# Optimization experiments

Measured on AMD Instinct MI355X. Metric: run time of the kernel, lower is better.

## Reference

```python
import jax, jax.numpy as jnp
import numpy as np
from jax import lax

B_, L_, D_MODEL, D_FF = 8, 1024, 512, 2048
D_STATE, D_CONV, EXPAND = 16, 4, 2
D_IN = EXPAND * D_MODEL
DT_RANK = (D_MODEL + 15) // 16  # 32


def _ln(x, g, b, eps=1e-5):
    m = jnp.mean(x, -1, keepdims=True)
    v = jnp.var(x, -1, keepdims=True)
    return (x - m) / jnp.sqrt(v + eps) * g + b


def _selective_scan(u, dt, A, Bm, Cm, D):
    # u, dt: (B,L,d_in); Bm, Cm: (B,L,d_state); A: (d_in,d_state); D: (d_in,)
    def step(h, xs):
        dt_t, B_t, C_t, u_t = xs  # (B,d_in),(B,ds),(B,ds),(B,d_in)
        dA = jnp.exp(dt_t[..., None] * A)                       # (B,d_in,ds)
        h = dA * h + (dt_t * u_t)[..., None] * B_t[:, None, :]  # (B,d_in,ds)
        y = jnp.einsum('bds,bs->bd', h, C_t)
        return h, y

    h0 = jnp.zeros((u.shape[0], D_IN, D_STATE), u.dtype)
    xs = (dt.transpose(1, 0, 2), Bm.transpose(1, 0, 2),
          Cm.transpose(1, 0, 2), u.transpose(1, 0, 2))
    _, ys = lax.scan(step, h0, xs)           # (L,B,d_in)
    return ys.transpose(1, 0, 2) + u * D


def _mamba(x, in_w, conv_w, conv_b, xp_w, dtp_w, dtp_b, A_log, D, out_w):
    xz = x @ in_w.T                              # (B,L,2*d_in)
    xs, z = jnp.split(xz, 2, axis=-1)
    # causal depthwise conv1d over L
    xc = lax.conv_general_dilated(xs.transpose(0, 2, 1), conv_w, (1,),
                                  [(D_CONV - 1, 0)], feature_group_count=D_IN)
    xc = jax.nn.silu(xc + conv_b[None, :, None]).transpose(0, 2, 1)  # (B,L,d_in)
    x_dbl = xc @ xp_w.T
    dt, Bm, Cm = jnp.split(x_dbl, [DT_RANK, DT_RANK + D_STATE], axis=-1)
    dt = jax.nn.softplus(dt @ dtp_w.T + dtp_b)
    A = -jnp.exp(A_log)
    y = _selective_scan(xc, dt, A, Bm, Cm, D)
    y = y * jax.nn.silu(z)
    return y @ out_w.T


def _forward(x,
             in1_w, conv1d1_w, conv1d1_b, xp1_w, dtp1_w, dtp1_b, Alog1, D1, outp1_w,
             in2_w, conv1d2_w, conv1d2_b, xp2_w, dtp2_w, dtp2_b, Alog2, D2, outp2_w,
             c1_w, c1_b, c2_w, c2_b, ln1_g, ln1_b, ln2_g, ln2_b):
    x_res = x  # dropout is identity in eval
    fwd = _mamba(x, in1_w, conv1d1_w, conv1d1_b, xp1_w, dtp1_w, dtp1_b, Alog1, D1, outp1_w)
    bwd = _mamba(jnp.flip(x, 1), in2_w, conv1d2_w, conv1d2_b, xp2_w, dtp2_w, dtp2_b,
                 Alog2, D2, outp2_w)
    new_x = fwd + jnp.flip(bwd, 1)
    x = _ln(new_x + x_res, ln1_g, ln1_b)
    y = jax.nn.gelu(jnp.einsum('bld,fd->blf', x, c1_w[:, :, 0]) + c1_b, approximate=False)
    y = jnp.einsum('blf,df->bld', y, c2_w[:, :, 0]) + c2_b
    return _ln(x + y, ln2_g, ln2_b)


def setup_inputs() -> dict:
    key = jax.random.key(0)
    ks = iter(jax.random.split(key, 32))
    rn = lambda shape, s=0.02: jax.random.normal(next(ks), shape, jnp.float32) * s

    def mamba_params():
        return dict(in_w=rn((2 * D_IN, D_MODEL)), conv_w=rn((D_IN, 1, D_CONV)),
                    conv_b=rn((D_IN,)), xp_w=rn((DT_RANK + 2 * D_STATE, D_IN)),
                    dtp_w=rn((D_IN, DT_RANK)), dtp_b=rn((D_IN,)),
                    A_log=jnp.log(jnp.tile(jnp.arange(1., D_STATE + 1.), (D_IN, 1))).astype(jnp.float32),
                    D=jnp.ones((D_IN,), jnp.float32), out_w=rn((D_MODEL, D_IN)))

    m1, m2 = mamba_params(), mamba_params()
    return {
        'x': jax.random.normal(next(ks), (B_, L_, D_MODEL), jnp.float32),
        'in1_w': m1['in_w'], 'conv1d1_w': m1['conv_w'], 'conv1d1_b': m1['conv_b'],
        'xp1_w': m1['xp_w'], 'dtp1_w': m1['dtp_w'], 'dtp1_b': m1['dtp_b'],
        'Alog1': m1['A_log'], 'D1': m1['D'], 'outp1_w': m1['out_w'],
        'in2_w': m2['in_w'], 'conv1d2_w': m2['conv_w'], 'conv1d2_b': m2['conv_b'],
        'xp2_w': m2['xp_w'], 'dtp2_w': m2['dtp_w'], 'dtp2_b': m2['dtp_b'],
        'Alog2': m2['A_log'], 'D2': m2['D'], 'outp2_w': m2['out_w'],
        'c1_w': rn((D_FF, D_MODEL, 1)), 'c1_b': rn((D_FF,)),
        'c2_w': rn((D_MODEL, D_FF, 1)), 'c2_b': rn((D_MODEL,)),
        'ln1_g': jnp.ones((D_MODEL,), jnp.float32), 'ln1_b': jnp.zeros((D_MODEL,), jnp.float32),
        'ln2_g': jnp.ones((D_MODEL,), jnp.float32), 'ln2_b': jnp.zeros((D_MODEL,), jnp.float32),
    }


def reference(x,
              in1_w, conv1d1_w, conv1d1_b, xp1_w, dtp1_w, dtp1_b, Alog1, D1, outp1_w,
              in2_w, conv1d2_w, conv1d2_b, xp2_w, dtp2_w, dtp2_b, Alog2, D2, outp2_w,
              c1_w, c1_b, c2_w, c2_b, ln1_g, ln1_b, ln2_g, ln2_b):
    return _forward(x,
                    in1_w, conv1d1_w, conv1d1_b, xp1_w, dtp1_w, dtp1_b, Alog1, D1, outp1_w,
                    in2_w, conv1d2_w, conv1d2_b, xp2_w, dtp2_w, dtp2_b, Alog2, D2, outp2_w,
                    c1_w, c1_b, c2_w, c2_b, ln1_g, ln1_b, ln2_g, ln2_b)
```

## Files before the change

kernel.cpp:

```cpp
#include <hip/hip_runtime.h>
#include <hip/hip_bf16.h>
#include <math.h>

#define B_SZ 8
#define L_SZ 1024
#define DM 512
#define DFF 2048
#define DIN 1024
#define DSTATE 16
#define DTRANK 32
#define MROWS (B_SZ * L_SZ)
#define CH 256
#define NCH 4

typedef __hip_bfloat16 bf16;
typedef unsigned short u16;
using f32x4 = __attribute__((ext_vector_type(4))) float;
using bfrag = __attribute__((ext_vector_type(8))) short;

__device__ inline float ldf(const float* p, long i) { return p[i]; }
__device__ inline float ldf(const bf16* p, long i) {
  return __uint_as_float((unsigned)((const u16*)p)[i] << 16);
}
__device__ inline void stf(float* p, long i, float v) { p[i] = v; }
__device__ inline void stf(bf16* p, long i, float v) { p[i] = __float2bfloat16(v); }
__device__ inline float b2f(u16 x) {
  return __uint_as_float((unsigned)x << 16);
}
__device__ inline u16 f2b(float v) {
  union { bf16 h; u16 u; } c;
  c.h = __float2bfloat16(v);
  return c.u;
}

__device__ inline float fexp2(float x) {
  float r;
  asm("v_exp_f32 %0, %1" : "=v"(r) : "v"(x));
  return r;
}

typedef __attribute__((address_space(1))) const void g_void;
typedef __attribute__((address_space(3))) void l_void;
__device__ inline void gl_lds16(const void* g, void* l) {
  __builtin_amdgcn_global_load_lds((g_void*)g, (l_void*)l, 16, 0, 0);
}

__device__ inline float4 ld4f_bt(const float* p) { return *(const float4*)p; }
__device__ inline float4 ld4f_bt(const bf16* p) {
  ushort4 u = *(const ushort4*)p;
  float4 v;
  v.x = b2f(u.x); v.y = b2f(u.y); v.z = b2f(u.z); v.w = b2f(u.w);
  return v;
}

__device__ inline void ld16f(const float* p, uint4& lo, uint4& hi) {
  float4 a = *(const float4*)p, b = *(const float4*)(p + 4);
  float4 c = *(const float4*)(p + 8), d = *(const float4*)(p + 12);
  union { uint4 v; u16 s[8]; } L, H;
  L.s[0] = f2b(a.x); L.s[1] = f2b(a.y); L.s[2] = f2b(a.z); L.s[3] = f2b(a.w);
  L.s[4] = f2b(b.x); L.s[5] = f2b(b.y); L.s[6] = f2b(b.z); L.s[7] = f2b(b.w);
  H.s[0] = f2b(c.x); H.s[1] = f2b(c.y); H.s[2] = f2b(c.z); H.s[3] = f2b(c.w);
  H.s[4] = f2b(d.x); H.s[5] = f2b(d.y); H.s[6] = f2b(d.z); H.s[7] = f2b(d.w);
  lo = L.v; hi = H.v;
}

__device__ inline float dpp_add_r8(float x) {
  float r; asm("v_add_f32 %0, %1, %2 row_ror:8" : "=v"(r) : "v"(x), "v"(x)); return r;
}
__device__ inline float dpp_add_r4(float x) {
  float r; asm("v_add_f32 %0, %1, %2 row_ror:4" : "=v"(r) : "v"(x), "v"(x)); return r;
}
__device__ inline float dpp_add_r2(float x) {
  float r; asm("v_add_f32 %0, %1, %2 row_ror:2" : "=v"(r) : "v"(x), "v"(x)); return r;
}
__device__ inline float dpp_add_r1(float x) {
  float r; asm("v_add_f32 %0, %1, %2 row_ror:1" : "=v"(r) : "v"(x), "v"(x)); return r;
}
__device__ inline float row16_sum(float x) {
  return dpp_add_r1(dpp_add_r2(dpp_add_r4(dpp_add_r8(x))));
}

__device__ inline int flipL(int r) {
  int t = r & (L_SZ - 1);
  return (r - t) + (L_SZ - 1 - t);
}

__global__ __launch_bounds__(256) void cvt8_k(
    const float* s0, const float* s1, const float* s2, const float* s3,
    const float* s4, const float* s5, const float* s6, const float* s7,
    bf16* d0, bf16* d1, bf16* d2, bf16* d3,
    bf16* d4, bf16* d5, bf16* d6, bf16* d7) {
  int blk = blockIdx.x;
  const float* s; bf16* d; long off;
  if (blk < 2048)       { s = s0; d = d0; off = (long)blk * 256; }
  else if (blk < 4096)  { s = s1; d = d1; off = (long)(blk - 2048) * 256; }
  else if (blk < 6144)  { s = s2; d = d2; off = (long)(blk - 4096) * 256; }
  else if (blk < 8192)  { s = s3; d = d3; off = (long)(blk - 6144) * 256; }
  else if (blk < 10240) { s = s4; d = d4; off = (long)(blk - 8192) * 256; }
  else if (blk < 12288) { s = s5; d = d5; off = (long)(blk - 10240) * 256; }
  else if (blk < 16384) { s = s6; d = d6; off = (long)(blk - 12288) * 256; }
  else                  { s = s7; d = d7; off = (long)(blk - 16384) * 256; }
  off += threadIdx.x;
  d[off] = __float2bfloat16(s[off]);
}

constexpr int MEPI_STORE2 = 0;
constexpr int MEPI_GATE2 = 1;
constexpr int MEPI_BIAS_GELU = 2;
constexpr int MEPI_BIAS_RES = 3;

template <int EPI, typename TA, typename TO>
__global__ __launch_bounds__(256) void mgemm_k(
    const TA* __restrict__ Ab, int lda,
    const bf16* __restrict__ Wb, int ldw,
    TO* __restrict__ C, TO* __restrict__ C2, int ldc,
    const float* __restrict__ bias,
    const float* __restrict__ res,
    int K) {
  constexpr bool ABF = (sizeof(TA) == 2);
  __shared__ u16 Wsm[128][32];
  __shared__ u16 AsmL[ABF ? 128 : 1][32];
  __shared__ u16 AsmP[ABF ? 1 : 128][ABF ? 1 : 40];
  const int tid = threadIdx.x;
  const int m0 = blockIdx.y * 128;
  const int n0 = blockIdx.x * 128;

  const int srow4 = tid >> 2;
  const int q16 = tid & 3;
  const u16* Wg0 = (const u16*)Wb + (long)(n0 + srow4) * ldw + q16 * 8;
  const u16* Wg1 = (const u16*)Wb + (long)(n0 + 64 + srow4) * ldw + q16 * 8;
  char* WsmB = (char*)&Wsm[0][0] + (tid >> 6) * 1024;

  const u16* Ag0 = (const u16*)Ab + (long)(m0 + srow4) * lda + q16 * 8;
  const u16* Ag1 = (const u16*)Ab + (long)(m0 + 64 + srow4) * lda + q16 * 8;
  char* AsmB = (char*)&AsmL[0][0] + (tid >> 6) * 1024;

  const int srow = tid >> 1;
  const int scol = (tid & 1) * 16;
  const TA* Agf = Ab + (long)(m0 + srow) * lda + scol;

  const int lane = tid & 63, quad = lane >> 4, l16 = lane & 15;
  const int wid = tid >> 6;
  const int wm = (wid & 1) * 64, wn = (wid >> 1) * 64;

  f32x4 acc[4][4];
#pragma unroll
  for (int i = 0; i < 4; ++i)
#pragma unroll
    for (int j = 0; j < 4; ++j) acc[i][j] = {0.f, 0.f, 0.f, 0.f};

  for (int k0 = 0; k0 < K; k0 += 32) {
    uint4 av0, av1;
    if constexpr (!ABF) ld16f((const float*)(Agf + k0), av0, av1);
    __syncthreads();
    gl_lds16(Wg0 + k0, WsmB);
    gl_lds16(Wg1 + k0, WsmB + 4096);
    if constexpr (ABF) {
      gl_lds16(Ag0 + k0, AsmB);
      gl_lds16(Ag1 + k0, AsmB + 4096);
    } else {
      *(uint4*)&AsmP[srow][scol] = av0;
      *(uint4*)&AsmP[srow][scol + 8] = av1;
    }
    __syncthreads();
    bfrag a[4], b[4];
#pragma unroll
    for (int mi = 0; mi < 4; ++mi) {
      if constexpr (ABF)
        a[mi] = *(const bfrag*)&AsmL[wm + mi * 16 + l16][quad * 8];
      else
        a[mi] = *(const bfrag*)&AsmP[wm + mi * 16 + l16][quad * 8];
    }
#pragma unroll
    for (int ni = 0; ni < 4; ++ni)
      b[ni] = *(const bfrag*)&Wsm[wn + ni * 16 + l16][quad * 8];
#pragma unroll
    for (int mi = 0; mi < 4; ++mi)
#pragma unroll
      for (int ni = 0; ni < 4; ++ni)
        acc[mi][ni] = __builtin_amdgcn_mfma_f32_16x16x32_bf16(
            a[mi], b[ni], acc[mi][ni], 0, 0, 0);
  }

  const bool second = (n0 >= DIN);
#pragma unroll
  for (int mi = 0; mi < 4; ++mi)
#pragma unroll
    for (int ni = 0; ni < 4; ++ni)
#pragma unroll
      for (int r = 0; r < 4; ++r) {
        int row = m0 + wm + mi * 16 + quad * 4 + r;
        int col = n0 + wn + ni * 16 + l16;
        float v = acc[mi][ni][r];
        if (EPI == MEPI_STORE2) {
          if (second) stf(C2, (long)flipL(row) * ldc + (col - DIN), v);
          else stf(C, (long)row * ldc + col, v);
        } else if (EPI == MEPI_GATE2) {
          TO* T = second ? C2 : C;
          long oi = second ? ((long)flipL(row) * ldc + (col - DIN))
                           : ((long)row * ldc + col);
          float y = ldf((const bf16*)T, oi);
          float sz = v / (1.f + __expf(-v));
          stf(T, oi, y * sz);
        } else if (EPI == MEPI_BIAS_GELU) {
          long oi = (long)row * ldc + col;
          v += bias[col];
          v = 0.5f * v * (1.f + erff(v * 0.70710678118654752440f));
          stf(C, oi, v);
        } else if (EPI == MEPI_BIAS_RES) {
          long oi = (long)row * ldc + col;
          ((float*)C)[oi] = v + bias[col] + res[oi];
        }
      }
}

__global__ __launch_bounds__(256) void mmerge_k(
    const bf16* __restrict__ y1, const bf16* __restrict__ y2,
    const bf16* __restrict__ W1, const bf16* __restrict__ W2,
    const float* __restrict__ xres, float* __restrict__ newx) {
  __shared__ u16 AsmL[128][32];
  __shared__ u16 Wsm[128][32];
  const int tid = threadIdx.x;
  const int m0 = blockIdx.y * 128;
  const int n0 = blockIdx.x * 128;

  const int srow4 = tid >> 2;
  const int q16 = tid & 3;
  int r1a = m0 + srow4, r1b = m0 + 64 + srow4;
  int r2a = flipL(r1a), r2b = flipL(r1b);
  const u16* A1g0 = (const u16*)y1 + (long)r1a * DIN + q16 * 8;
  const u16* A1g1 = (const u16*)y1 + (long)r1b * DIN + q16 * 8;
  const u16* A2g0 = (const u16*)y2 + (long)r2a * DIN + q16 * 8;
  const u16* A2g1 = (const u16*)y2 + (long)r2b * DIN + q16 * 8;
  const u16* W1g0 = (const u16*)W1 + (long)(n0 + srow4) * DIN + q16 * 8;
  const u16* W1g1 = (const u16*)W1 + (long)(n0 + 64 + srow4) * DIN + q16 * 8;
  const u16* W2g0 = (const u16*)W2 + (long)(n0 + srow4) * DIN + q16 * 8;
  const u16* W2g1 = (const u16*)W2 + (long)(n0 + 64 + srow4) * DIN + q16 * 8;
  char* AsmB = (char*)&AsmL[0][0] + (tid >> 6) * 1024;
  char* WsmB = (char*)&Wsm[0][0] + (tid >> 6) * 1024;

  const int lane = tid & 63, quad = lane >> 4, l16 = lane & 15;
  const int wid = tid >> 6;
  const int wm = (wid & 1) * 64, wn = (wid >> 1) * 64;

  f32x4 acc[4][4];
#pragma unroll
  for (int i = 0; i < 4; ++i)
#pragma unroll
    for (int j = 0; j < 4; ++j) acc[i][j] = {0.f, 0.f, 0.f, 0.f};

  for (int k0 = 0; k0 < 2 * DIN; k0 += 32) {
    const bool ph2 = (k0 >= DIN);
    const int kk = k0 & (DIN - 1);
    const u16* a0 = ph2 ? A2g0 : A1g0;
    const u16* a1 = ph2 ? A2g1 : A1g1;
    const u16* w0 = ph2 ? W2g0 : W1g0;
    const u16* w1 = ph2 ? W2g1 : W1g1;
    __syncthreads();
    gl_lds16(a0 + kk, AsmB);
    gl_lds16(a1 + kk, AsmB + 4096);
    gl_lds16(w0 + kk, WsmB);
    gl_lds16(w1 + kk, WsmB + 4096);
    __syncthreads();
    bfrag a[4], b[4];
#pragma unroll
    for (int mi = 0; mi < 4; ++mi)
      a[mi] = *(const bfrag*)&AsmL[wm + mi * 16 + l16][quad * 8];
#pragma unroll
    for (int ni = 0; ni < 4; ++ni)
      b[ni] = *(const bfrag*)&Wsm[wn + ni * 16 + l16][quad * 8];
#pragma unroll
    for (int mi = 0; mi < 4; ++mi)
#pragma unroll
      for (int ni = 0; ni < 4; ++ni)
        acc[mi][ni] = __builtin_amdgcn_mfma_f32_16x16x32_bf16(
            a[mi], b[ni], acc[mi][ni], 0, 0, 0);
  }

#pragma unroll
  for (int mi = 0; mi < 4; ++mi)
#pragma unroll
    for (int ni = 0; ni < 4; ++ni)
#pragma unroll
      for (int r = 0; r < 4; ++r) {
        int row = m0 + wm + mi * 16 + quad * 4 + r;
        int col = n0 + wn + ni * 16 + l16;
        long oi = (long)row * DM + col;
        newx[oi] = acc[mi][ni][r] + xres[oi];
      }
}

constexpr int EPI_NONE = 0;
constexpr int EPI_SOFTPLUS_ROW = 1;

#define BM 64
#define BN 64
#define BKK 16

template <int EPI, typename TB, typename TO>
__global__ __launch_bounds__(256) void gemmBT_k(
    const float* __restrict__ A,
    const TB* __restrict__ B,
    TO* __restrict__ C, int N,
    const float* __restrict__ bias, int K) {
  __shared__ float As[BKK][BM + 4];
  __shared__ float Bs[BKK][BN + 4];
  const int tid = threadIdx.x;
  const int m0 = blockIdx.y * BM;
  const int n0 = blockIdx.x * BN;
  const int tx = tid & 15;
  const int ty = tid >> 4;
  const int lrow = tid >> 2;
  const int lcol = (tid & 3) * 4;
  const int kr = tid >> 4;
  const int nc = (tid & 15) * 4;

  const float* Arow = A + (long)(m0 + lrow) * K;

  float acc[4][4] = {};
  for (int k0 = 0; k0 < K; k0 += BKK) {
    float4 av = *(const float4*)(Arow + k0 + lcol);
    float4 bv = ld4f_bt(B + (long)(k0 + kr) * N + n0 + nc);
    As[lcol + 0][lrow] = av.x; As[lcol + 1][lrow] = av.y;
    As[lcol + 2][lrow] = av.z; As[lcol + 3][lrow] = av.w;
    Bs[kr][nc + 0] = bv.x; Bs[kr][nc + 1] = bv.y;
    Bs[kr][nc + 2] = bv.z; Bs[kr][nc + 3] = bv.w;
    __syncthreads();
#pragma unroll
    for (int k = 0; k < BKK; ++k) {
      float a[4], b[4];
#pragma unroll
      for (int i = 0; i < 4; ++i) a[i] = As[k][ty * 4 + i];
#pragma unroll
      for (int j = 0; j < 4; ++j) b[j] = Bs[k][tx * 4 + j];
#pragma unroll
      for (int i = 0; i < 4; ++i)
#pragma unroll
        for (int j = 0; j < 4; ++j) acc[i][j] += a[i] * b[j];
    }
    __syncthreads();
  }

#pragma unroll
  for (int i = 0; i < 4; ++i) {
    int r = m0 + ty * 4 + i;
#pragma unroll
    for (int j = 0; j < 4; ++j) {
      int c = n0 + tx * 4 + j;
      float v = acc[i][j];
      if (EPI == EPI_SOFTPLUS_ROW) {
        v += bias[r];
        v = (v > 20.f) ? v : log1pf(__expf(v));
      }
      stf(C, (long)r * N + c, v);
    }
  }
}

#define XSLICE 4
#define XSZ ((long)64 * MROWS)

__global__ __launch_bounds__(256) void xprojs_k(
    const float* __restrict__ A1, const bf16* __restrict__ B1,
    float* __restrict__ P1,
    const float* __restrict__ A2, const bf16* __restrict__ B2,
    float* __restrict__ P2) {
  __shared__ float As[BKK][BM + 4];
  __shared__ float Bs[BKK][BN + 4];
  const int tid = threadIdx.x;
  const int n0 = blockIdx.x * BN;
  const int slice = blockIdx.y;
  const int kbeg = slice * (DIN / XSLICE);
  const int dir = blockIdx.z;
  const float* A = dir ? A2 : A1;
  const bf16* Bm = dir ? B2 : B1;
  float* P = (dir ? P2 : P1) + (long)slice * XSZ;
  const int N = MROWS, K = DIN;
  const int tx = tid & 15;
  const int ty = tid >> 4;
  const int lrow = tid >> 2;
  const int lcol = (tid & 3) * 4;
  const int kr = tid >> 4;
  const int nc = (tid & 15) * 4;

  const float* Arow = A + (long)lrow * K;

  float acc[4][4] = {};
  for (int k0 = kbeg; k0 < kbeg + DIN / XSLICE; k0 += BKK) {
    float4 av = *(const float4*)(Arow + k0 + lcol);
    float4 bv = ld4f_bt(Bm + (long)(k0 + kr) * N + n0 + nc);
    As[lcol + 0][lrow] = av.x; As[lcol + 1][lrow] = av.y;
    As[lcol + 2][lrow] = av.z; As[lcol + 3][lrow] = av.w;
    Bs[kr][nc + 0] = bv.x; Bs[kr][nc + 1] = bv.y;
    Bs[kr][nc + 2] = bv.z; Bs[kr][nc + 3] = bv.w;
    __syncthreads();
#pragma unroll
    for (int k = 0; k < BKK; ++k) {
      float a[4], b[4];
#pragma unroll
      for (int i = 0; i < 4; ++i) a[i] = As[k][ty * 4 + i];
#pragma unroll
      for (int j = 0; j < 4; ++j) b[j] = Bs[k][tx * 4 + j];
#pragma unroll
      for (int i = 0; i < 4; ++i)
#pragma unroll
        for (int j = 0; j < 4; ++j) acc[i][j] += a[i] * b[j];
    }
    __syncthreads();
  }

#pragma unroll
  for (int i = 0; i < 4; ++i) {
    int r = ty * 4 + i;
#pragma unroll
    for (int j = 0; j < 4; ++j) {
      int c = n0 + tx * 4 + j;
      P[(long)r * N + c] = acc[i][j];
    }
  }
}

__global__ __launch_bounds__(256) void xred_k(
    const float* __restrict__ P1, float* __restrict__ o1,
    const float* __restrict__ P2, float* __restrict__ o2) {
  long i = (long)blockIdx.x * 256 + threadIdx.x;
  const float* P = blockIdx.y ? P2 : P1;
  float* o = blockIdx.y ? o2 : o1;
  o[i] = P[i] + P[i + XSZ] + P[i + 2 * XSZ] + P[i + 3 * XSZ];
}

__global__ __launch_bounds__(256) void convT_k(
    const bf16* __restrict__ xs, const float* __restrict__ w,
    const float* __restrict__ b, bf16* __restrict__ xcT) {
  __shared__ u16 T[64][72];
  int c0 = blockIdx.x * 64;
  int r0 = blockIdx.y * 64;
  int tid = threadIdx.x;
  int tr = tid >> 2;
  int tc = (tid & 3) * 16;

  const u16* src = (const u16*)xs + (long)(r0 + tr) * DIN + c0 + tc;
  uint4 v0 = *(const uint4*)src;
  uint4 v1 = *(const uint4*)(src + 8);
  u16 tmp[16];
  *(uint4*)tmp = v0;
  *(uint4*)(tmp + 8) = v1;
#pragma unroll
  for (int j = 0; j < 16; ++j) T[tc + j][tr + 3] = tmp[j];
  bool head = (r0 & (L_SZ - 1)) == 0;
  if (tid < 12) {
    int hr = tid >> 2;
    int seg = (tid & 3) * 16;
    if (head) {
#pragma unroll
      for (int j = 0; j < 16; ++j) T[seg + j][hr] = 0;
    } else {
      const u16* hs = (const u16*)xs + (long)(r0 - 3 + hr) * DIN + c0 + seg;
      uint4 h0 = *(const uint4*)hs;
      uint4 h1 = *(const uint4*)(hs + 8);
      u16 ht[16];
      *(uint4*)ht = h0;
      *(uint4*)(ht + 8) = h1;
#pragma unroll
      for (int j = 0; j < 16; ++j) T[seg + j][hr] = ht[j];
    }
  }
  __syncthreads();

  int d = c0 + tr;
  float w0 = w[d * 4 + 0], w1 = w[d * 4 + 1], w2 = w[d * 4 + 2], w3 = w[d * 4 + 3];
  float bd = b[d];
  float X[19];
#pragma unroll
  for (int k = 0; k < 19; ++k) X[k] = b2f(T[tr][tc + k]);
  u16 o[16];
#pragma unroll
  for (int j = 0; j < 16; ++j) {
    float acc = bd + w0 * X[j] + w1 * X[j + 1] + w2 * X[j + 2] + w3 * X[j + 3];
    o[j] = f2b(acc / (1.f + __expf(-acc)));
  }
  u16* dst = (u16*)xcT + (long)d * MROWS + r0 + tc;
  *(uint4*)dst = *(uint4*)o;
  *(uint4*)(dst + 8) = *(uint4*)(o + 8);
}

__global__ __launch_bounds__(256, 4) void scan1_k(
    const u16* __restrict__ dtT1, const u16* __restrict__ dtT2,
    const u16* __restrict__ uT1, const u16* __restrict__ uT2,
    const float* __restrict__ xd1, const float* __restrict__ xd2,
    const float* __restrict__ Alog1, const float* __restrict__ Alog2,
    bf16* __restrict__ hl1, bf16* __restrict__ hl2,
    float* __restrict__ sd1, float* __restrict__ sd2) {
  int blk = blockIdx.x;
  int dblk = blk & 15;
  int r = blk >> 4;
  int c = r % 3; r /= 3;
  int b = r & 7;
  int dir = r >> 3;
  int tid = threadIdx.x;
  int s = tid & 15;
  int gi = tid >> 4;
  int d0 = dblk * 64 + gi * 4;
  const u16* dtT = dir ? dtT2 : dtT1;
  const u16* uT = dir ? uT2 : uT1;
  const float* xd = dir ? xd2 : xd1;
  const float* Alog = dir ? Alog2 : Alog1;
  bf16* hl = dir ? hl2 : hl1;
  float* sd = dir ? sd2 : sd1;

  float A2[4], h[4], sdt[4];
#pragma unroll
  for (int dd = 0; dd < 4; ++dd) {
    A2[dd] = -__expf(Alog[(d0 + dd) * DSTATE + s]) * 1.4426950408889634f;
    h[dd] = 0.f;
    sdt[dd] = 0.f;
  }
  long t0 = (long)b * L_SZ + c * CH;
  const u16* pdt = dtT + (long)d0 * MROWS + t0;
  const u16* pu = uT + (long)d0 * MROWS + t0;
  const float* pB = xd + (long)(DTRANK + s) * MROWS + t0;

  for (int g = 0; g < CH / 8; ++g) {
    union { uint4 v; u16 a[8]; } dt8[4], u8[4];
    union { float4 v[2]; float a[8]; } B8;
#pragma unroll
    for (int dd = 0; dd < 4; ++dd) {
      dt8[dd].v = *(const uint4*)(pdt + (long)dd * MROWS + g * 8);
      u8[dd].v = *(const uint4*)(pu + (long)dd * MROWS + g * 8);
    }
    B8.v[0] = *(const float4*)(pB + g * 8);
    B8.v[1] = *(const float4*)(pB + g * 8 + 4);
#pragma unroll
    for (int j = 0; j < 8; ++j) {
      float Bj = B8.a[j];
#pragma unroll
      for (int dd = 0; dd < 4; ++dd) {
        float dtv = b2f(dt8[dd].a[j]);
        float uv = b2f(u8[dd].a[j]);
        float da = fexp2(dtv * A2[dd]);
        h[dd] = da * h[dd] + (dtv * uv) * Bj;
        sdt[dd] += dtv;
      }
    }
  }
#pragma unroll
  for (int dd = 0; dd < 4; ++dd) {
    int ci = (b * 3 + c) * 1024 + d0 + dd;
    hl[(long)ci * 16 + s] = __float2bfloat16(h[dd]);
    if (s == 0) sd[ci] = sdt[dd];
  }
}

__global__ __launch_bounds__(256, 4) void scan2_k(
    const u16* __restrict__ dtT1, const u16* __restrict__ dtT2,
    const u16* __restrict__ uT1, const u16* __restrict__ uT2,
    const float* __restrict__ xd1, const float* __restrict__ xd2,
    const float* __restrict__ Alog1, const float* __restrict__ Alog2,
    const float* __restrict__ D1, const float* __restrict__ D2,
    const bf16* __restrict__ hl1, const bf16* __restrict__ hl2,
    const float* __restrict__ sd1, const float* __restrict__ sd2,
    bf16* __restrict__ y1, bf16* __restrict__ y2) {
  int blk = blockIdx.x;
  int dblk = blk & 15;
  int c = (blk >> 4) & 3;
  int b = (blk >> 6) & 7;
  int dir = blk >> 9;
  int tid = threadIdx.x;
  int s = tid & 15;
  int gi = tid >> 4;
  int d0 = dblk * 64 + gi * 4;
  const u16* dtT = dir ? dtT2 : dtT1;
  const u16* uT = dir ? uT2 : uT1;
  const float* xd = dir ? xd2 : xd1;
  const float* Alog = dir ? Alog2 : Alog1;
  const float* Dp = dir ? D2 : D1;
  const bf16* hl = dir ? hl2 : hl1;
  const float* sd = dir ? sd2 : sd1;
  bf16* out = dir ? y2 : y1;

  float A2[4], h[4], Dd[4];
#pragma unroll
  for (int dd = 0; dd < 4; ++dd) {
    A2[dd] = -__expf(Alog[(d0 + dd) * DSTATE + s]) * 1.4426950408889634f;
    Dd[dd] = Dp[d0 + dd];
    h[dd] = 0.f;
  }

  for (int cc = 0; cc < c; ++cc) {
#pragma unroll
    for (int dd = 0; dd < 4; ++dd) {
      int ci = (b * 3 + cc) * 1024 + d0 + dd;
      float P = fexp2(A2[dd] * sd[ci]);
      h[dd] = h[dd] * P + b2f(((const u16*)hl)[(long)ci * 16 + s]);
    }
  }

  long t0 = (long)b * L_SZ + c * CH;
  const u16* pdt = dtT + (long)d0 * MROWS + t0;
  const u16* pu = uT + (long)d0 * MROWS + t0;
  const float* pB = xd + (long)(DTRANK + s) * MROWS + t0;
  const float* pC = xd + (long)(DTRANK + DSTATE + s) * MROWS + t0;
  u16* outb = (u16*)out + (long)b * L_SZ * DIN + (long)c * CH * DIN + d0;

  for (int g = 0; g < CH / 8; ++g) {
    union { uint4 v; u16 a[8]; } dt8[4], u8[4];
    union { float4 v[2]; float a[8]; } B8, C8;
#pragma unroll
    for (int dd = 0; dd < 4; ++dd) {
      dt8[dd].v = *(const uint4*)(pdt + (long)dd * MROWS + g * 8);
      u8[dd].v = *(const uint4*)(pu + (long)dd * MROWS + g * 8);
    }
    B8.v[0] = *(const float4*)(pB + g * 8);
    B8.v[1] = *(const float4*)(pB + g * 8 + 4);
    C8.v[0] = *(const float4*)(pC + g * 8);
    C8.v[1] = *(const float4*)(pC + g * 8 + 4);
    u16* og = outb + (long)g * 8 * DIN;
#pragma unroll
    for (int j = 0; j < 8; ++j) {
      float Bj = B8.a[j];
      float Cj = C8.a[j];
      u16 o4[4];
#pragma unroll
      for (int dd = 0; dd < 4; ++dd) {
        float dtv = b2f(dt8[dd].a[j]);
        float uv = b2f(u8[dd].a[j]);
        float da = fexp2(dtv * A2[dd]);
        h[dd] = da * h[dd] + (dtv * uv) * Bj;
        float q = row16_sum(h[dd] * Cj);
        o4[dd] = f2b(q + Dd[dd] * uv);
      }
      if (s == 0) *(uint2*)(og + (long)j * DIN) = *(uint2*)o4;
    }
  }
}

__global__ __launch_bounds__(256) void ln_k(
    const float* __restrict__ xin, const float* __restrict__ g,
    const float* __restrict__ bb, float* __restrict__ out,
    bf16* __restrict__ outb) {
  int row = blockIdx.x;
  const float* p = xin + (long)row * DM;
  int tid = threadIdx.x;
  float x0 = p[tid], x1 = p[tid + 256];
  float sum = x0 + x1;
  float sq = x0 * x0 + x1 * x1;
#pragma unroll
  for (int o = 1; o < 64; o <<= 1) {
    sum += __shfl_xor(sum, o, 64);
    sq += __shfl_xor(sq, o, 64);
  }
  __shared__ float ssum[4], ssq[4];
  int wv = tid >> 6;
  if ((tid & 63) == 0) { ssum[wv] = sum; ssq[wv] = sq; }
  __syncthreads();
  sum = ssum[0] + ssum[1] + ssum[2] + ssum[3];
  sq = ssq[0] + ssq[1] + ssq[2] + ssq[3];
  float mean = sum * (1.f / DM);
  float var = sq * (1.f / DM) - mean * mean;
  float rstd = rsqrtf(var + 1e-5f);
  float v0 = (x0 - mean) * rstd * g[tid] + bb[tid];
  float v1 = (x1 - mean) * rstd * g[tid + 256] + bb[tid + 256];
  out[(long)row * DM + tid] = v0;
  out[(long)row * DM + tid + 256] = v1;
  if (outb) {
    stf(outb, (long)row * DM + tid, v0);
    stf(outb, (long)row * DM + tid + 256, v1);
  }
}

extern "C" void kernel_launch(void* const* d_in, const int* in_sizes, int n_in,
                              void* d_out, int out_size, void* d_ws, size_t ws_size,
                              hipStream_t stream) {
  const float* x = (const float*)d_in[0];
  const float* in1_w = (const float*)d_in[1];
  const float* conv1_w = (const float*)d_in[2];
  const float* conv1_b = (const float*)d_in[3];
  const float* xp1_w = (const float*)d_in[4];
  const float* dtp1_w = (const float*)d_in[5];
  const float* dtp1_b = (const float*)d_in[6];
  const float* Alog1 = (const float*)d_in[7];
  const float* D1 = (const float*)d_in[8];
  const float* outp1_w = (const float*)d_in[9];
  const float* in2_w = (const float*)d_in[10];
  const float* conv2_w = (const float*)d_in[11];
  const float* conv2_b = (const float*)d_in[12];
  const float* xp2_w = (const float*)d_in[13];
  const float* dtp2_w = (const float*)d_in[14];
  const float* dtp2_b = (const float*)d_in[15];
  const float* Alog2 = (const float*)d_in[16];
  const float* D2 = (const float*)d_in[17];
  const float* outp2_w = (const float*)d_in[18];
  const float* c1_w = (const float*)d_in[19];
  const float* c1_b = (const float*)d_in[20];
  const float* c2_w = (const float*)d_in[21];
  const float* c2_b = (const float*)d_in[22];
  const float* ln1_g = (const float*)d_in[23];
  const float* ln1_b = (const float*)d_in[24];
  const float* ln2_g = (const float*)d_in[25];
  const float* ln2_b = (const float*)d_in[26];

  const long MB = 1024L * 1024;
  char* wsb = (char*)d_ws;
  bf16* A = (bf16*)(wsb + 0 * MB);
  bf16* B = (bf16*)(wsb + 16 * MB);
  bf16* C = (bf16*)(wsb + 32 * MB);
  bf16* D = (bf16*)(wsb + 48 * MB);
  bf16* E = (bf16*)(wsb + 64 * MB);
  bf16* F = (bf16*)(wsb + 80 * MB);
  float* Bf = (float*)B;
  float* Cf = (float*)C;
  float* Af = (float*)A;
  bf16* ffn = C;
  float* P1 = (float*)A;
  float* P2 = (float*)D;

  char* ob = (char*)d_out;
  bf16* Wxs = (bf16*)(ob + 0 * MB);
  bf16* Wg = (bf16*)(ob + 2 * MB);
  bf16* o1b = (bf16*)(ob + 4 * MB);
  bf16* o2b = (bf16*)(ob + 5 * MB);
  bf16* c1b = (bf16*)(ob + 6 * MB);
  bf16* c2b = (bf16*)(ob + 8 * MB);
  float* xdT1 = (float*)(ob + 10 * MB);
  float* xdT2 = (float*)(ob + 12 * MB);
  float* sd1 = (float*)(ob + 14 * MB);
  float* sd2 = (float*)(ob + 14 * MB + 131072);
  bf16* hl1 = (bf16*)(ob + 14 * MB + 262144);
  bf16* hl2 = (bf16*)(ob + 15 * MB);

  const long HWN = (long)DIN * DM;

  dim3 blk(256);
  dim3 gP2(2 * DIN / 128, MROWS / 128);
  dim3 gM(DM / 128, MROWS / 128);
  dim3 gF(DFF / 128, MROWS / 128);
  dim3 gC(DIN / 64, MROWS / 64);
  dim3 gXs(MROWS / BN, XSLICE, 2);
  dim3 gXr(XSZ / 256, 2);
  dim3 gD(MROWS / BN, DIN / BM);

  cvt8_k<<<20480, blk, 0, stream>>>(
      in1_w, in2_w, in1_w + HWN, in2_w + HWN, outp1_w, outp2_w, c1_w, c2_w,
      Wxs, Wxs + HWN, Wg, Wg + HWN, o1b, o2b, c1b, c2b);

  mgemm_k<MEPI_STORE2, float, bf16><<<gP2, blk, 0, stream>>>(
      x, DM, Wxs, DM, A, D, DIN, nullptr, nullptr, DM);

  convT_k<<<gC, blk, 0, stream>>>(A, conv1_w, conv1_b, B);
  convT_k<<<gC, blk, 0, stream>>>(D, conv2_w, conv2_b, E);

  xprojs_k<<<gXs, blk, 0, stream>>>(xp1_w, B, P1, xp2_w, E, P2);
  xred_k<<<gXr, blk, 0, stream>>>(P1, xdT1, P2, xdT2);

  gemmBT_k<EPI_SOFTPLUS_ROW, float, bf16><<<gD, blk, 0, stream>>>(
      dtp1_w, xdT1, C, MROWS, dtp1_b, DTRANK);
  gemmBT_k<EPI_SOFTPLUS_ROW, float, bf16><<<gD, blk, 0, stream>>>(
      dtp2_w, xdT2, F, MROWS, dtp2_b, DTRANK);

  scan1_k<<<2 * 8 * 3 * 16, blk, 0, stream>>>(
      (const u16*)C, (const u16*)F, (const u16*)B, (const u16*)E,
      xdT1, xdT2, Alog1, Alog2, hl1, hl2, sd1, sd2);
  scan2_k<<<2 * 8 * 4 * 16, blk, 0, stream>>>(
      (const u16*)C, (const u16*)F, (const u16*)B, (const u16*)E,
      xdT1, xdT2, Alog1, Alog2, D1, D2, hl1, hl2, sd1, sd2, A, D);

  mgemm_k<MEPI_GATE2, float, bf16><<<gP2, blk, 0, stream>>>(
      x, DM, Wg, DM, A, D, DIN, nullptr, nullptr, DM);

  mmerge_k<<<gM, blk, 0, stream>>>(A, D, o1b, o2b, x, Cf);

  ln_k<<<MROWS, blk, 0, stream>>>(Cf, ln1_g, ln1_b, Bf, E);

  mgemm_k<MEPI_BIAS_GELU, bf16, bf16><<<gF, blk, 0, stream>>>(
      E, DM, c1b, DM, ffn, nullptr, DFF, c1_b, nullptr, DM);
  mgemm_k<MEPI_BIAS_RES, bf16, float><<<gM, blk, 0, stream>>>(
      ffn, DFF, c2b, DFF, Af, nullptr, DM, c2_b, Bf, DFF);

  ln_k<<<MROWS, blk, 0, stream>>>(Af, ln2_g, ln2_b, (float*)d_out, nullptr);
}
```

Before: 726.5 us.

## Pre-convert x to bf16, merge per-direction conv and dt-proj launches

The input x is now converted to bf16 once, inside the weight-conversion kernel and again before the gate GEMM, so mgemm always takes bf16 A through direct global-to-LDS loads instead of converting fp32 in registers. The two conv kernels are merged into one launch with a direction grid dimension. The generic fp32 dt-projection GEMM is replaced by a specialised kernel covering both directions that keeps the weights in LDS and writes 8 bf16 outputs per row. This removes launches and conversion work from the GEMM inner loops, at the cost of an extra conversion pass and extra bf16 buffer traffic.

```diff
diff --git a/kernel.cpp b/kernel.cpp
--- a/kernel.cpp
+++ b/kernel.cpp
@@ -53,17 +53,6 @@
   return v;
 }
 
-__device__ inline void ld16f(const float* p, uint4& lo, uint4& hi) {
-  float4 a = *(const float4*)p, b = *(const float4*)(p + 4);
-  float4 c = *(const float4*)(p + 8), d = *(const float4*)(p + 12);
-  union { uint4 v; u16 s[8]; } L, H;
-  L.s[0] = f2b(a.x); L.s[1] = f2b(a.y); L.s[2] = f2b(a.z); L.s[3] = f2b(a.w);
-  L.s[4] = f2b(b.x); L.s[5] = f2b(b.y); L.s[6] = f2b(b.z); L.s[7] = f2b(b.w);
-  H.s[0] = f2b(c.x); H.s[1] = f2b(c.y); H.s[2] = f2b(c.z); H.s[3] = f2b(c.w);
-  H.s[4] = f2b(d.x); H.s[5] = f2b(d.y); H.s[6] = f2b(d.z); H.s[7] = f2b(d.w);
-  lo = L.v; hi = H.v;
-}
-
 __device__ inline float dpp_add_r8(float x) {
   float r; asm("v_add_f32 %0, %1, %2 row_ror:8" : "=v"(r) : "v"(x), "v"(x)); return r;
 }
@@ -85,11 +74,18 @@
   return (r - t) + (L_SZ - 1 - t);
 }
 
-__global__ __launch_bounds__(256) void cvt8_k(
+__global__ __launch_bounds__(256) void cvt_k(const float* __restrict__ s,
+                                             bf16* __restrict__ d, int n) {
+  int i = blockIdx.x * 256 + threadIdx.x;
+  if (i < n) d[i] = __float2bfloat16(s[i]);
+}
+
+__global__ __launch_bounds__(256) void cvt9_k(
     const float* s0, const float* s1, const float* s2, const float* s3,
     const float* s4, const float* s5, const float* s6, const float* s7,
+    const float* s8,
     bf16* d0, bf16* d1, bf16* d2, bf16* d3,
-    bf16* d4, bf16* d5, bf16* d6, bf16* d7) {
+    bf16* d4, bf16* d5, bf16* d6, bf16* d7, bf16* d8) {
   int blk = blockIdx.x;
   const float* s; bf16* d; long off;
   if (blk < 2048)       { s = s0; d = d0; off = (long)blk * 256; }
@@ -99,7 +95,8 @@
   else if (blk < 10240) { s = s4; d = d4; off = (long)(blk - 8192) * 256; }
   else if (blk < 12288) { s = s5; d = d5; off = (long)(blk - 10240) * 256; }
   else if (blk < 16384) { s = s6; d = d6; off = (long)(blk - 12288) * 256; }
-  else                  { s = s7; d = d7; off = (long)(blk - 16384) * 256; }
+  else if (blk < 20480) { s = s7; d = d7; off = (long)(blk - 16384) * 256; }
+  else                  { s = s8; d = d8; off = (long)(blk - 20480) * 256; }
   off += threadIdx.x;
   d[off] = __float2bfloat16(s[off]);
 }
@@ -109,18 +106,16 @@
 constexpr int MEPI_BIAS_GELU = 2;
 constexpr int MEPI_BIAS_RES = 3;
 
-template <int EPI, typename TA, typename TO>
+template <int EPI, typename TO>
 __global__ __launch_bounds__(256) void mgemm_k(
-    const TA* __restrict__ Ab, int lda,
+    const bf16* __restrict__ Ab, int lda,
     const bf16* __restrict__ Wb, int ldw,
     TO* __restrict__ C, TO* __restrict__ C2, int ldc,
     const float* __restrict__ bias,
     const float* __restrict__ res,
     int K) {
-  constexpr bool ABF = (sizeof(TA) == 2);
   __shared__ u16 Wsm[128][32];
-  __shared__ u16 AsmL[ABF ? 128 : 1][32];
-  __shared__ u16 AsmP[ABF ? 1 : 128][ABF ? 1 : 40];
+  __shared__ u16 AsmL[128][32];
   const int tid = threadIdx.x;
   const int m0 = blockIdx.y * 128;
   const int n0 = blockIdx.x * 128;
@@ -135,10 +130,6 @@
   const u16* Ag1 = (const u16*)Ab + (long)(m0 + 64 + srow4) * lda + q16 * 8;
   char* AsmB = (char*)&AsmL[0][0] + (tid >> 6) * 1024;
 
-  const int srow = tid >> 1;
-  const int scol = (tid & 1) * 16;
-  const TA* Agf = Ab + (long)(m0 + srow) * lda + scol;
-
   const int lane = tid & 63, quad = lane >> 4, l16 = lane & 15;
   const int wid = tid >> 6;
   const int wm = (wid & 1) * 64, wn = (wid >> 1) * 64;
@@ -150,27 +141,16 @@
     for (int j = 0; j < 4; ++j) acc[i][j] = {0.f, 0.f, 0.f, 0.f};
 
   for (int k0 = 0; k0 < K; k0 += 32) {
-    uint4 av0, av1;
-    if constexpr (!ABF) ld16f((const float*)(Agf + k0), av0, av1);
     __syncthreads();
     gl_lds16(Wg0 + k0, WsmB);
     gl_lds16(Wg1 + k0, WsmB + 4096);
-    if constexpr (ABF) {
-      gl_lds16(Ag0 + k0, AsmB);
-      gl_lds16(Ag1 + k0, AsmB + 4096);
-    } else {
-      *(uint4*)&AsmP[srow][scol] = av0;
-      *(uint4*)&AsmP[srow][scol + 8] = av1;
-    }
+    gl_lds16(Ag0 + k0, AsmB);
+    gl_lds16(Ag1 + k0, AsmB + 4096);
     __syncthreads();
     bfrag a[4], b[4];
 #pragma unroll
-    for (int mi = 0; mi < 4; ++mi) {
-      if constexpr (ABF)
-        a[mi] = *(const bfrag*)&AsmL[wm + mi * 16 + l16][quad * 8];
-      else
-        a[mi] = *(const bfrag*)&AsmP[wm + mi * 16 + l16][quad * 8];
-    }
+    for (int mi = 0; mi < 4; ++mi)
+      a[mi] = *(const bfrag*)&AsmL[wm + mi * 16 + l16][quad * 8];
 #pragma unroll
     for (int ni = 0; ni < 4; ++ni)
       b[ni] = *(const bfrag*)&Wsm[wn + ni * 16 + l16][quad * 8];
@@ -290,73 +270,70 @@
       }
 }
 
-constexpr int EPI_NONE = 0;
-constexpr int EPI_SOFTPLUS_ROW = 1;
+__global__ __launch_bounds__(256) void dtT2_k(
+    const float* __restrict__ A1, const float* __restrict__ A2,
+    const float* __restrict__ B1, const float* __restrict__ B2,
+    bf16* __restrict__ C1, bf16* __restrict__ C2,
+    const float* __restrict__ bias1, const float* __restrict__ bias2) {
+  __shared__ float Ws[64][33];
+  __shared__ float Bi[64];
+  const int tid = threadIdx.x;
+  const int c0 = blockIdx.x * 128;
+  const int r0 = blockIdx.y * 64;
+  const int dir = blockIdx.z;
+  const float* A = dir ? A2 : A1;
+  const float* B = dir ? B2 : B1;
+  bf16* C = dir ? C2 : C1;
+  const float* bias = dir ? bias2 : bias1;
+
+  {
+    int wr = tid >> 2, wc = (tid & 3) * 8;
+    const float* src = A + (long)(r0 + wr) * DTRANK + wc;
+    float4 v0 = *(const float4*)src;
+    float4 v1 = *(const float4*)(src + 4);
+    Ws[wr][wc + 0] = v0.x; Ws[wr][wc + 1] = v0.y;
+    Ws[wr][wc + 2] = v0.z; Ws[wr][wc + 3] = v0.w;
+    Ws[wr][wc + 4] = v1.x; Ws[wr][wc + 5] = v1.y;
+    Ws[wr][wc + 6] = v1.z; Ws[wr][wc + 7] = v1.w;
+    if (tid < 64) Bi[tid] = bias[r0 + tid];
+  }
+  __syncthreads();
+
+  const int rg = tid >> 4;
+  const int cx = (tid & 15) * 8;
+  const float* pb = B + c0 + cx;
+
+  float acc[4][8] = {};
+  for (int k = 0; k < DTRANK; ++k) {
+    float4 b0 = *(const float4*)(pb + (long)k * MROWS);
+    float4 b1 = *(const float4*)(pb + (long)k * MROWS + 4);
+    float bb[8] = {b0.x, b0.y, b0.z, b0.w, b1.x, b1.y, b1.z, b1.w};
+#pragma unroll
+    for (int i = 0; i < 4; ++i) {
+      float w = Ws[rg * 4 + i][k];
+#pragma unroll
+      for (int j = 0; j < 8; ++j) acc[i][j] += w * bb[j];
+    }
+  }
+
+#pragma unroll
+  for (int i = 0; i < 4; ++i) {
+    int r = r0 + rg * 4 + i;
+    float bs = Bi[rg * 4 + i];
+    u16 o8[8];
+#pragma unroll
+    for (int j = 0; j < 8; ++j) {
+      float v = acc[i][j] + bs;
+      v = (v > 20.f) ? v : log1pf(__expf(v));
+      o8[j] = f2b(v);
+    }
+    *(uint4*)((u16*)C + (long)r * MROWS + c0 + cx) = *(uint4*)o8;
+  }
+}
 
 #define BM 64
 #define BN 64
 #define BKK 16
-
-template <int EPI, typename TB, typename TO>
-__global__ __launch_bounds__(256) void gemmBT_k(
-    const float* __restrict__ A,
-    const TB* __restrict__ B,
-    TO* __restrict__ C, int N,
-    const float* __restrict__ bias, int K) {
-  __shared__ float As[BKK][BM + 4];
-  __shared__ float Bs[BKK][BN + 4];
-  const int tid = threadIdx.x;
-  const int m0 = blockIdx.y * BM;
-  const int n0 = blockIdx.x * BN;
-  const int tx = tid & 15;
-  const int ty = tid >> 4;
-  const int lrow = tid >> 2;
-  const int lcol = (tid & 3) * 4;
-  const int kr = tid >> 4;
-  const int nc = (tid & 15) * 4;
-
-  const float* Arow = A + (long)(m0 + lrow) * K;
-
-  float acc[4][4] = {};
-  for (int k0 = 0; k0 < K; k0 += BKK) {
-    float4 av = *(const float4*)(Arow + k0 + lcol);
-    float4 bv = ld4f_bt(B + (long)(k0 + kr) * N + n0 + nc);
-    As[lcol + 0][lrow] = av.x; As[lcol + 1][lrow] = av.y;
-    As[lcol + 2][lrow] = av.z; As[lcol + 3][lrow] = av.w;
-    Bs[kr][nc + 0] = bv.x; Bs[kr][nc + 1] = bv.y;
-    Bs[kr][nc + 2] = bv.z; Bs[kr][nc + 3] = bv.w;
-    __syncthreads();
-#pragma unroll
-    for (int k = 0; k < BKK; ++k) {
-      float a[4], b[4];
-#pragma unroll
-      for (int i = 0; i < 4; ++i) a[i] = As[k][ty * 4 + i];
-#pragma unroll
-      for (int j = 0; j < 4; ++j) b[j] = Bs[k][tx * 4 + j];
-#pragma unroll
-      for (int i = 0; i < 4; ++i)
-#pragma unroll
-        for (int j = 0; j < 4; ++j) acc[i][j] += a[i] * b[j];
-    }
-    __syncthreads();
-  }
-
-#pragma unroll
-  for (int i = 0; i < 4; ++i) {
-    int r = m0 + ty * 4 + i;
-#pragma unroll
-    for (int j = 0; j < 4; ++j) {
-      int c = n0 + tx * 4 + j;
-      float v = acc[i][j];
-      if (EPI == EPI_SOFTPLUS_ROW) {
-        v += bias[r];
-        v = (v > 20.f) ? v : log1pf(__expf(v));
-      }
-      stf(C, (long)r * N + c, v);
-    }
-  }
-}
-
 #define XSLICE 4
 #define XSZ ((long)64 * MROWS)
 
@@ -429,12 +406,19 @@
   o[i] = P[i] + P[i + XSZ] + P[i + 2 * XSZ] + P[i + 3 * XSZ];
 }
 
-__global__ __launch_bounds__(256) void convT_k(
-    const bf16* __restrict__ xs, const float* __restrict__ w,
-    const float* __restrict__ b, bf16* __restrict__ xcT) {
+__global__ __launch_bounds__(256) void convT2_k(
+    const bf16* __restrict__ xs1, const bf16* __restrict__ xs2,
+    const float* __restrict__ w1, const float* __restrict__ w2,
+    const float* __restrict__ b1, const float* __restrict__ b2,
+    bf16* __restrict__ o1, bf16* __restrict__ o2) {
   __shared__ u16 T[64][72];
   int c0 = blockIdx.x * 64;
   int r0 = blockIdx.y * 64;
+  int dir = blockIdx.z;
+  const bf16* xs = dir ? xs2 : xs1;
+  const float* w = dir ? w2 : w1;
+  const float* b = dir ? b2 : b1;
+  bf16* xcT = dir ? o2 : o1;
   int tid = threadIdx.x;
   int tr = tid >> 2;
   int tc = (tid & 3) * 16;
@@ -468,7 +452,7 @@
   __syncthreads();
 
   int d = c0 + tr;
-  float w0 = w[d * 4 + 0], w1 = w[d * 4 + 1], w2 = w[d * 4 + 2], w3 = w[d * 4 + 3];
+  float w0 = w[d * 4 + 0], wq1 = w[d * 4 + 1], wq2 = w[d * 4 + 2], wq3 = w[d * 4 + 3];
   float bd = b[d];
   float X[19];
 #pragma unroll
@@ -476,7 +460,7 @@
   u16 o[16];
 #pragma unroll
   for (int j = 0; j < 16; ++j) {
-    float acc = bd + w0 * X[j] + w1 * X[j + 1] + w2 * X[j + 2] + w3 * X[j + 3];
+    float acc = bd + w0 * X[j] + wq1 * X[j + 1] + wq2 * X[j + 2] + wq3 * X[j + 3];
     o[j] = f2b(acc / (1.f + __expf(-acc)));
   }
   u16* dst = (u16*)xcT + (long)d * MROWS + r0 + tc;
@@ -713,6 +697,8 @@
   bf16* ffn = C;
   float* P1 = (float*)A;
   float* P2 = (float*)D;
+  bf16* xb = B;
+  bf16* xb2 = F;
 
   char* ob = (char*)d_out;
   bf16* Wxs = (bf16*)(ob + 0 * MB);
@@ -734,28 +720,26 @@
   dim3 gP2(2 * DIN / 128, MROWS / 128);
   dim3 gM(DM / 128, MROWS / 128);
   dim3 gF(DFF / 128, MROWS / 128);
-  dim3 gC(DIN / 64, MROWS / 64);
+  dim3 gC2(DIN / 64, MROWS / 64, 2);
   dim3 gXs(MROWS / BN, XSLICE, 2);
   dim3 gXr(XSZ / 256, 2);
-  dim3 gD(MROWS / BN, DIN / BM);
-
-  cvt8_k<<<20480, blk, 0, stream>>>(
-      in1_w, in2_w, in1_w + HWN, in2_w + HWN, outp1_w, outp2_w, c1_w, c2_w,
-      Wxs, Wxs + HWN, Wg, Wg + HWN, o1b, o2b, c1b, c2b);
-
-  mgemm_k<MEPI_STORE2, float, bf16><<<gP2, blk, 0, stream>>>(
-      x, DM, Wxs, DM, A, D, DIN, nullptr, nullptr, DM);
-
-  convT_k<<<gC, blk, 0, stream>>>(A, conv1_w, conv1_b, B);
-  convT_k<<<gC, blk, 0, stream>>>(D, conv2_w, conv2_b, E);
+  dim3 gDt(MROWS / 128, 1024 / 64, 2);
+
+  cvt9_k<<<36864, blk, 0, stream>>>(
+      in1_w, in2_w, in1_w + HWN, in2_w + HWN, outp1_w, outp2_w, c1_w, c2_w, x,
+      Wxs, Wxs + HWN, Wg, Wg + HWN, o1b, o2b, c1b, c2b, xb);
+
+  mgemm_k<MEPI_STORE2, bf16><<<gP2, blk, 0, stream>>>(
+      xb, DM, Wxs, DM, A, D, DIN, nullptr, nullptr, DM);
+
+  convT2_k<<<gC2, blk, 0, stream>>>(A, D, conv1_w, conv2_w, conv1_b, conv2_b,
+                                    B, E);
 
   xprojs_k<<<gXs, blk, 0, stream>>>(xp1_w, B, P1, xp2_w, E, P2);
   xred_k<<<gXr, blk, 0, stream>>>(P1, xdT1, P2, xdT2);
 
-  gemmBT_k<EPI_SOFTPLUS_ROW, float, bf16><<<gD, blk, 0, stream>>>(
-      dtp1_w, xdT1, C, MROWS, dtp1_b, DTRANK);
-  gemmBT_k<EPI_SOFTPLUS_ROW, float, bf16><<<gD, blk, 0, stream>>>(
-      dtp2_w, xdT2, F, MROWS, dtp2_b, DTRANK);
+  dtT2_k<<<gDt, blk, 0, stream>>>(dtp1_w, dtp2_w, xdT1, xdT2, C, F,
+                                  dtp1_b, dtp2_b);
 
   scan1_k<<<2 * 8 * 3 * 16, blk, 0, stream>>>(
       (const u16*)C, (const u16*)F, (const u16*)B, (const u16*)E,
@@ -764,16 +748,17 @@
       (const u16*)C, (const u16*)F, (const u16*)B, (const u16*)E,
       xdT1, xdT2, Alog1, Alog2, D1, D2, hl1, hl2, sd1, sd2, A, D);
 
-  mgemm_k<MEPI_GATE2, float, bf16><<<gP2, blk, 0, stream>>>(
-      x, DM, Wg, DM, A, D, DIN, nullptr, nullptr, DM);
+  cvt_k<<<(MROWS * DM) / 256, blk, 0, stream>>>(x, xb2, MROWS * DM);
+  mgemm_k<MEPI_GATE2, bf16><<<gP2, blk, 0, stream>>>(
+      xb2, DM, Wg, DM, A, D, DIN, nullptr, nullptr, DM);
 
   mmerge_k<<<gM, blk, 0, stream>>>(A, D, o1b, o2b, x, Cf);
 
   ln_k<<<MROWS, blk, 0, stream>>>(Cf, ln1_g, ln1_b, Bf, E);
 
-  mgemm_k<MEPI_BIAS_GELU, bf16, bf16><<<gF, blk, 0, stream>>>(
+  mgemm_k<MEPI_BIAS_GELU, bf16><<<gF, blk, 0, stream>>>(
       E, DM, c1b, DM, ffn, nullptr, DFF, c1_b, nullptr, DM);
-  mgemm_k<MEPI_BIAS_RES, bf16, float><<<gM, blk, 0, stream>>>(
+  mgemm_k<MEPI_BIAS_RES, float><<<gM, blk, 0, stream>>>(
       ffn, DFF, c2b, DFF, Af, nullptr, DM, c2_b, Bf, DFF);
 
   ln_k<<<MROWS, blk, 0, stream>>>(Af, ln2_g, ln2_b, (float*)d_out, nullptr);
```

After: 935.1 us. +28.7%, slower.
